# Performance work log

Hardware: AMD Instinct MI355X
Metric: run time of the kernel (lower is better)

## Reference

```python
import math
import jax, jax.numpy as jnp
import numpy as np

L, H = 4, 8  # num_layers, num_heads
SPARSE_FACTOR = 0.1
NEG = -1e9


def _ln(x, g, b, eps=1e-5):
    m = jnp.mean(x, axis=-1, keepdims=True)
    v = jnp.mean(jnp.square(x - m), axis=-1, keepdims=True)
    return (x - m) * jax.lax.rsqrt(v + eps) * g + b


def _pos_enc(S, D):
    # sinusoidal PE, shape (S, 1, D) matching pe.unsqueeze(0).transpose(0,1)[:S]
    pos = np.arange(S, dtype=np.float32)[:, None]
    div = np.exp(np.arange(0, D, 2, dtype=np.float32) * (-math.log(10000.0) / D))
    pe = np.zeros((S, D), dtype=np.float32)
    pe[:, 0::2] = np.sin(pos * div)
    pe[:, 1::2] = np.cos(pos * div)
    return jnp.asarray(pe)[:, None, :]


def setup_inputs() -> dict:
    key = jax.random.key(0)
    B, S, I, D, F = 128, 512, 64, 512, 2048
    ks = jax.random.split(key, 10)
    w = lambda k, shape: jax.random.normal(k, shape, jnp.float32) * 0.02
    return {
        'x': jax.random.normal(ks[0], (B, S, I), jnp.float32),
        'W_in': w(ks[1], (I, D)), 'b_in': jnp.zeros((D,), jnp.float32),
        'ln1_g': jnp.ones((L, D), jnp.float32), 'ln1_b': jnp.zeros((L, D), jnp.float32),
        'Wq': w(ks[2], (L, D, D)), 'Wk': w(ks[3], (L, D, D)), 'Wv': w(ks[4], (L, D, D)),
        'Wo': w(ks[5], (L, D, D)), 'bo': jnp.zeros((L, D), jnp.float32),
        'ln2_g': jnp.ones((L, D), jnp.float32), 'ln2_b': jnp.zeros((L, D), jnp.float32),
        'W1': w(ks[6], (L, D, F)), 'b1': jnp.zeros((L, F), jnp.float32),
        'W2': w(ks[7], (L, F, D)), 'b2': jnp.zeros((L, D), jnp.float32),
        'lnf_g': jnp.ones((D,), jnp.float32), 'lnf_b': jnp.zeros((D,), jnp.float32),
    }


def reference(x, W_in, b_in, ln1_g, ln1_b, Wq, Wk, Wv, Wo, bo,
              ln2_g, ln2_b, W1, b1, W2, b2, lnf_g, lnf_b):
    B, S, _ = x.shape
    D = W_in.shape[1]
    dk = D // H
    # source: scores last dim == batch (view+transpose quirk); k = max(1, int(B*0.1))
    topk = max(1, int(B * SPARSE_FACTOR))
    h = jnp.swapaxes(x, 0, 1) @ W_in + b_in          # (S,B,D)
    h = h * math.sqrt(D) + _pos_enc(S, D)

    def heads(z, w):
        return jnp.swapaxes((z @ w).reshape(S, B, H, dk), 1, 2)  # (S,H,B,dk)

    def body(h, p):
        g1, bb1, wq, wk, wv, wo, bo_, g2, bb2, w1, b1_, w2, b2_ = p
        y = _ln(h, g1, bb1)
        q, k, v = heads(y, wq), heads(y, wk), heads(y, wv)
        scores = jnp.einsum('shbd,shcd->shbc', q, k) / math.sqrt(dk)  # (S,H,B,B)
        kth = jax.lax.top_k(scores, topk)[0][..., -1:]
        scores = jnp.where(scores >= kth, scores, NEG)  # top-k sparsification
        attn = jax.nn.softmax(scores, axis=-1)
        ctx = jnp.einsum('shbc,shcd->shbd', attn, v)
        ctx = jnp.swapaxes(ctx, 1, 2).reshape(S, B, D)
        h = ctx @ wo + bo_ + h                       # attn out + residual
        f = jax.nn.gelu(_ln(h, g2, bb2) @ w1 + b1_, approximate=False) @ w2 + b2_
        return h + f, None

    h, _ = jax.lax.scan(body, h, (ln1_g, ln1_b, Wq, Wk, Wv, Wo, bo,
                                  ln2_g, ln2_b, W1, b1, W2, b2))
    h = _ln(h, lnf_g, lnf_b)
    return jnp.swapaxes(h, 0, 1)                     # (B,S,D)
```

## Files before the change

kernel.cpp:

```cpp
#include <hip/hip_runtime.h>
#include <math.h>

#define S_ 512
#define B_ 128
#define D_ 512
#define I_ 64
#define F_ 2048
#define H_ 8
#define DK_ 64
#define L_ 4
#define SB_ (S_*B_)

typedef unsigned short u16;
typedef unsigned int u32;
typedef __attribute__((ext_vector_type(4))) unsigned int u32x4;
typedef __attribute__((ext_vector_type(4))) float f32x4;

__device__ __forceinline__ u16 f2bf(float f){
  u32 x = __builtin_bit_cast(u32, f);
  x += 0x7fffu + ((x >> 16) & 1u);
  return (u16)(x >> 16);
}

__device__ __forceinline__ void mfma16(f32x4& c, const u32x4& a, const u32x4& b){
  asm volatile("v_mfma_f32_16x16x32_bf16 %0, %1, %2, %0" : "+v"(c) : "v"(a), "v"(b));
}

__device__ __forceinline__ void gload16(const u16* g, u16* l){
  __builtin_amdgcn_global_load_lds((const __attribute__((address_space(1))) unsigned int*)g,
                                   (__attribute__((address_space(3))) unsigned int*)l, 16, 0, 0);
}

__global__ void pe_kernel(float* __restrict__ pe){
  int s = blockIdx.x, d = threadIdx.x;
  float e = expf((float)(d & ~1) * (-9.210340371976184f / (float)D_));
  float arg = (float)s * e;
  pe[s*D_ + d] = (d & 1) ? cosf(arg) : sinf(arg);
}

__global__ void transpose_bf16(const float* __restrict__ src, u16* __restrict__ dst,
                               int R, int C, size_t zstride){
  __shared__ float t[32][33];
  size_t sbase = (size_t)blockIdx.z * R * C;
  size_t dbase = (size_t)blockIdx.z * zstride;
  int r0 = blockIdx.y*32, c0 = blockIdx.x*32;
  int tx = threadIdx.x, ty = threadIdx.y;
  #pragma unroll
  for (int j=0;j<4;j++)
    t[ty+j*8][tx] = src[sbase + (size_t)(r0+ty+j*8)*C + c0+tx];
  __syncthreads();
  #pragma unroll
  for (int j=0;j<4;j++)
    dst[dbase + (size_t)(c0+ty+j*8)*R + r0+tx] = f2bf(t[tx][ty+j*8]);
}

__global__ __launch_bounds__(512) void inproj_kernel(const float* __restrict__ x,
    const float* __restrict__ Win, const float* __restrict__ bin,
    const float* __restrict__ pe, float* __restrict__ h){
  __shared__ float xs[8][64];
  int t = threadIdx.x;
  float w[64];
  #pragma unroll
  for (int i=0;i<64;i++) w[i] = Win[i*D_ + t];
  float bd = bin[t];
  int r0 = blockIdx.x * 128;
  for (int batch=0; batch<16; batch++){
    int rb = r0 + batch*8;
    {
      int rr = t >> 6, i = t & 63;
      int r = rb + rr;
      int s = r >> 7, b = r & 127;
      xs[rr][i] = x[((size_t)b*S_ + s)*I_ + i];
    }
    __syncthreads();
    float acc[8];
    #pragma unroll
    for (int rr=0;rr<8;rr++) acc[rr] = 0.f;
    #pragma unroll
    for (int i4=0;i4<16;i4++){
      f32x4 xv[8];
      #pragma unroll
      for (int rr=0;rr<8;rr++) xv[rr] = *(const f32x4*)&xs[rr][i4*4];
      #pragma unroll
      for (int rr=0;rr<8;rr++){
        acc[rr] = fmaf(xv[rr][0], w[i4*4+0], acc[rr]);
        acc[rr] = fmaf(xv[rr][1], w[i4*4+1], acc[rr]);
        acc[rr] = fmaf(xv[rr][2], w[i4*4+2], acc[rr]);
        acc[rr] = fmaf(xv[rr][3], w[i4*4+3], acc[rr]);
      }
    }
    #pragma unroll
    for (int rr=0;rr<8;rr++){
      int r = rb + rr;
      int s = r >> 7;
      h[(size_t)r*D_ + t] = (acc[rr] + bd) * 22.627416997969522f + pe[s*D_ + t];
    }
    __syncthreads();
  }
}

template<int FINAL>
__global__ __launch_bounds__(256) void ln_kernel(const float* __restrict__ hsrc,
    const float* __restrict__ g, const float* __restrict__ bb,
    u16* __restrict__ outb, float* __restrict__ outf){
  int row = blockIdx.x*4 + (threadIdx.x>>6);
  int lane = threadIdx.x & 63;
  const float* hr = hsrc + (size_t)row*D_ + lane*8;
  f32x4 a0 = *(const f32x4*)hr;
  f32x4 a1 = *(const f32x4*)(hr+4);
  float v[8];
  #pragma unroll
  for (int j=0;j<4;j++){ v[j]=a0[j]; v[4+j]=a1[j]; }
  float sum = 0.f;
  #pragma unroll
  for (int j=0;j<8;j++) sum += v[j];
  #pragma unroll
  for (int m=1;m<64;m<<=1) sum += __shfl_xor(sum, m);
  float mean = sum * (1.f/(float)D_);
  float s2 = 0.f;
  #pragma unroll
  for (int j=0;j<8;j++){ float dd = v[j]-mean; s2 = fmaf(dd,dd,s2); }
  #pragma unroll
  for (int m=1;m<64;m<<=1) s2 += __shfl_xor(s2, m);
  float inv = rsqrtf(s2*(1.f/(float)D_) + 1e-5f);
  f32x4 g0 = *(const f32x4*)&g[lane*8];
  f32x4 g1 = *(const f32x4*)&g[lane*8+4];
  f32x4 b0 = *(const f32x4*)&bb[lane*8];
  f32x4 b1 = *(const f32x4*)&bb[lane*8+4];
  float o[8];
  #pragma unroll
  for (int j=0;j<4;j++){
    o[j]   = (v[j]-mean)*inv*g0[j] + b0[j];
    o[4+j] = (v[4+j]-mean)*inv*g1[j] + b1[j];
  }
  if (FINAL == 0){
    u32x4 pk;
    #pragma unroll
    for (int j=0;j<4;j++)
      pk[j] = (u32)f2bf(o[2*j]) | ((u32)f2bf(o[2*j+1])<<16);
    *(u32x4*)&outb[(size_t)row*D_ + lane*8] = pk;
  } else {
    int s = row>>7, b = row&(B_-1);
    float* op = outf + ((size_t)b*S_ + s)*D_ + lane*8;
    f32x4 r0, r1;
    #pragma unroll
    for (int j=0;j<4;j++){ r0[j]=o[j]; r1[j]=o[4+j]; }
    *(f32x4*)op = r0;
    *(f32x4*)(op+4) = r1;
  }
}

template<int MODE>
__global__ __launch_bounds__(256) void gemm_kernel(const u16* __restrict__ A,
    const u16* __restrict__ Wt, const float* __restrict__ bias,
    float* __restrict__ hres, u16* __restrict__ outb, int N, int K){
  const u32 nwg = gridDim.x * gridDim.y;
  u32 wg = blockIdx.y * gridDim.x + blockIdx.x;
  wg = (wg & 7) * (nwg >> 3) + (wg >> 3);
  const int m0 = (int)(wg / gridDim.x) * 128;
  const int n0 = (int)(wg % gridDim.x) * 128;
  __shared__ u16 a_lds[128*32];
  __shared__ u16 b_lds[128*32];
  const int t = threadIdx.x;
  const int lane = t & 63, wave = t >> 6;
  const int wm = wave >> 1, wn = wave & 1;
  const int rsel = lane & 15, kg = (lane>>4)*8;
  const u16* ag = A  + (size_t)(m0 + (t>>2))*K + (t&3)*8;
  const u16* bg = Wt + (size_t)(n0 + (t>>2))*K + (t&3)*8;
  f32x4 acc[4][4] = {};
  for (int k0 = 0; k0 < K; k0 += 32){
    asm volatile("s_nop 7\n\ts_nop 7");
    __syncthreads();
    gload16(ag + k0,                &a_lds[t*8]);
    gload16(ag + 64*(size_t)K + k0, &a_lds[2048 + t*8]);
    gload16(bg + k0,                &b_lds[t*8]);
    gload16(bg + 64*(size_t)K + k0, &b_lds[2048 + t*8]);
    __syncthreads();
    u32x4 af[4], bfr[4];
    #pragma unroll
    for (int i=0;i<4;i++){
      af[i]  = *(const u32x4*)&a_lds[(wm*64 + i*16 + rsel)*32 + kg];
      bfr[i] = *(const u32x4*)&b_lds[(wn*64 + i*16 + rsel)*32 + kg];
    }
    #pragma unroll
    for (int i=0;i<4;i++)
      #pragma unroll
      for (int j=0;j<4;j++)
        mfma16(acc[i][j], af[i], bfr[j]);
  }
  asm volatile("s_nop 7\n\ts_nop 7");
  const int rb = (lane>>4)*4;
  #pragma unroll
  for (int i=0;i<4;i++){
    #pragma unroll
    for (int j=0;j<4;j++){
      int gn = n0 + wn*64 + j*16 + rsel;
      #pragma unroll
      for (int rg=0;rg<4;rg++){
        int gr = m0 + wm*64 + i*16 + rb + rg;
        float val = acc[i][j][rg];
        if (MODE == 0){
          int mat = gn >> 9;
          int hh = (gn >> 6) & 7, dd = gn & 63;
          int s = gr >> 7, b = gr & 127;
          u16* dst = outb + (size_t)mat*33554432ull;
          dst[(size_t)((s*H_ + hh)*B_ + b)*DK_ + dd] = f2bf(val);
        } else if (MODE == 1){
          hres[(size_t)gr*D_ + gn] += val + bias[gn];
        } else {
          float xg = val + bias[gn];
          float ge = 0.5f*xg*(1.f + erff(xg*0.7071067811865476f));
          outb[(size_t)gr*(size_t)N + gn] = f2bf(ge);
        }
      }
    }
  }
}

__global__ __launch_bounds__(256, 2) void attn_kernel(const u16* __restrict__ qb,
    const u16* __restrict__ kb, const u16* __restrict__ vb, u16* __restrict__ cb){
  __shared__ __align__(16) char smem[80384];
  u16* q_lds = (u16*)smem;
  u16* k_lds = (u16*)(smem + 18432);
  float* S   = (float*)smem;
  u16* P     = (u16*)smem;
  u16* vT    = (u16*)(smem + 34816);
  u32* wl    = (u32*)(smem + 67584);
  float* rs  = (float*)(smem + 79872);
  int sh = blockIdx.x;
  int s = sh >> 3, hh = sh & 7;
  int t = threadIdx.x, lane = t & 63, wave = t >> 6;
  const u16* qg = qb + (size_t)sh * (B_*DK_);
  const u16* kg = kb + (size_t)sh * (B_*DK_);
  const u16* vg = vb + (size_t)sh * (B_*DK_);
  #pragma unroll
  for (int rr=0; rr<4; rr++){
    int idx = rr*2048 + t*8;
    int row = idx >> 6, col = idx & 63;
    *(u32x4*)&q_lds[row*72+col] = *(const u32x4*)&qg[idx];
    *(u32x4*)&k_lds[row*72+col] = *(const u32x4*)&kg[idx];
  }
  __syncthreads();
  int wm = wave>>1, wn = wave&1, rsel = lane & 15;
  f32x4 sacc[4][4] = {};
  #pragma unroll
  for (int ks=0; ks<2; ks++){
    asm volatile("s_nop 7\n\ts_nop 7");
    int ko = ks*32 + (lane>>4)*8;
    u32x4 qf[4], kf[4];
    #pragma unroll
    for (int i=0;i<4;i++){
      qf[i] = *(const u32x4*)&q_lds[(wm*64+i*16+rsel)*72 + ko];
      kf[i] = *(const u32x4*)&k_lds[(wn*64+i*16+rsel)*72 + ko];
    }
    #pragma unroll
    for (int i=0;i<4;i++)
      #pragma unroll
      for (int j=0;j<4;j++)
        mfma16(sacc[i][j], qf[i], kf[j]);
  }
  asm volatile("s_nop 7\n\ts_nop 7");
  __syncthreads();
  int rb = (lane>>4)*4;
  #pragma unroll
  for (int i=0;i<4;i++)
    #pragma unroll
    for (int j=0;j<4;j++)
      #pragma unroll
      for (int rg=0;rg<4;rg++)
        S[(wm*64+i*16+rb+rg)*132 + wn*64+j*16+rsel] = sacc[i][j][rg] * 0.125f;
  __syncthreads();
  int r = t >> 1, half = t & 1;
  const f32x4* srow4 = (const f32x4*)(S + r*132 + half*64);
  float kv[12];
  #pragma unroll
  for (int i=0;i<12;i++) kv[i] = -3.4e38f;
  for (int i4=0;i4<16;i4++){
    f32x4 v4 = srow4[i4];
    float m4 = fmaxf(fmaxf(v4[0],v4[1]), fmaxf(v4[2],v4[3]));
    if (m4 > kv[11]){
      #pragma unroll
      for (int z=0; z<4; z++){
        float inc = v4[z];
        if (inc > kv[11]){
          #pragma unroll
          for (int p=0;p<12;p++){
            float cur = kv[p];
            bool gt = inc > cur;
            kv[p] = gt ? inc : cur;
            inc   = gt ? cur : inc;
          }
        }
      }
    }
  }
  float kth = 3.4e38f;
  #pragma unroll
  for (int i=0;i<12;i++){
    float pb = __shfl_xor(kv[11-i], 1);
    kth = fminf(kth, fmaxf(kv[i], pb));
  }
  float mx = fmaxf(kv[0], __shfl_xor(kv[0], 1));
  float sum = 0.f;
  int n = 0;
  u32* myw = wl + t*12;
  for (int i4=0;i4<16;i4++){
    f32x4 v4 = srow4[i4];
    #pragma unroll
    for (int z=0; z<4; z++){
      float v = v4[z];
      if (v >= kth && n < 12){
        float e = __expf(v - mx);
        sum += e;
        myw[n] = ((u32)f2bf(e) << 16) | (u32)(half*64 + i4*4 + z);
        n++;
      }
    }
  }
  float tsum = sum + __shfl_xor(sum, 1);
  if (!half) rs[r] = 1.f / tsum;
  __syncthreads();
  {
    u32x4 zz = {0u,0u,0u,0u};
    #pragma unroll
    for (int z=0; z<9; z++){
      int idx = z*256 + t;
      if (idx < 2176) ((u32x4*)P)[idx] = zz;
    }
  }
  #pragma unroll
  for (int rr=0; rr<16; rr++){
    int idx2 = (rr*256 + t)*2;
    u32 u = *(const u32*)&vg[idx2];
    int c = idx2 >> 6, d0 = idx2 & 63;
    vT[d0*136 + c]     = (u16)(u & 0xffffu);
    vT[(d0+1)*136 + c] = (u16)(u >> 16);
  }
  __syncthreads();
  u16* prow = P + r*136;
  for (int j=0; j<n; j++){
    u32 e = myw[j];
    prow[e & 0xffffu] = (u16)(e >> 16);
  }
  __syncthreads();
  f32x4 cacc[4][2] = {};
  #pragma unroll
  for (int ks=0; ks<4; ks++){
    asm volatile("s_nop 7\n\ts_nop 7");
    int ko = ks*32 + (lane>>4)*8;
    u32x4 pf[4], vf[2];
    #pragma unroll
    for (int i=0;i<4;i++) pf[i] = *(const u32x4*)&P[(wm*64+i*16+rsel)*136 + ko];
    #pragma unroll
    for (int j=0;j<2;j++) vf[j] = *(const u32x4*)&vT[(wn*32+j*16+rsel)*136 + ko];
    #pragma unroll
    for (int i=0;i<4;i++)
      #pragma unroll
      for (int j=0;j<2;j++)
        mfma16(cacc[i][j], pf[i], vf[j]);
  }
  asm volatile("s_nop 7\n\ts_nop 7");
  #pragma unroll
  for (int i=0;i<4;i++)
    #pragma unroll
    for (int j=0;j<2;j++)
      #pragma unroll
      for (int rg=0;rg<4;rg++){
        int m = wm*64 + i*16 + rb + rg;
        int nn = wn*32 + j*16 + rsel;
        float val = cacc[i][j][rg] * rs[m];
        cb[((size_t)(s*B_ + m))*D_ + hh*DK_ + nn] = f2bf(val);
      }
}

extern "C" void kernel_launch(void* const* d_in, const int* in_sizes, int n_in,
                              void* d_out, int out_size, void* d_ws, size_t ws_size,
                              hipStream_t stream) {
  const float* x    = (const float*)d_in[0];
  const float* Win  = (const float*)d_in[1];
  const float* bin  = (const float*)d_in[2];
  const float* ln1g = (const float*)d_in[3];
  const float* ln1b = (const float*)d_in[4];
  const float* Wq   = (const float*)d_in[5];
  const float* Wk   = (const float*)d_in[6];
  const float* Wv   = (const float*)d_in[7];
  const float* Wo   = (const float*)d_in[8];
  const float* bo   = (const float*)d_in[9];
  const float* ln2g = (const float*)d_in[10];
  const float* ln2b = (const float*)d_in[11];
  const float* W1   = (const float*)d_in[12];
  const float* b1   = (const float*)d_in[13];
  const float* W2   = (const float*)d_in[14];
  const float* b2   = (const float*)d_in[15];
  const float* lnfg = (const float*)d_in[16];
  const float* lnfb = (const float*)d_in[17];

  char* ws = (char*)d_ws;
  float* h  = (float*)(ws);
  u16* yb   = (u16*)(ws + 134217728ull);
  u16* qb   = (u16*)(ws + 201326592ull);
  u16* kb   = (u16*)(ws + 268435456ull);
  u16* vb   = (u16*)(ws + 335544320ull);
  u16* cb   = (u16*)(ws + 402653184ull);
  u16* act  = qb;
  u16* wqkvT= (u16*)(ws + 469762048ull);
  u16* woT  = (u16*)(ws + 476053504ull);
  u16* w1T  = (u16*)(ws + 478150656ull);
  u16* w2T  = (u16*)(ws + 486539264ull);
  float* pe = (float*)(ws + 494927872ull);

  dim3 tb(32,8);
  pe_kernel<<<S_, D_, 0, stream>>>(pe);
  transpose_bf16<<<dim3(D_/32, D_/32, L_), tb, 0, stream>>>(Wq, wqkvT,            D_, D_, (size_t)3*D_*D_);
  transpose_bf16<<<dim3(D_/32, D_/32, L_), tb, 0, stream>>>(Wk, wqkvT + D_*D_,    D_, D_, (size_t)3*D_*D_);
  transpose_bf16<<<dim3(D_/32, D_/32, L_), tb, 0, stream>>>(Wv, wqkvT + 2*D_*D_,  D_, D_, (size_t)3*D_*D_);
  transpose_bf16<<<dim3(D_/32, D_/32, L_), tb, 0, stream>>>(Wo, woT,              D_, D_, (size_t)D_*D_);
  transpose_bf16<<<dim3(F_/32, D_/32, L_), tb, 0, stream>>>(W1, w1T, D_, F_, (size_t)D_*F_);
  transpose_bf16<<<dim3(D_/32, F_/32, L_), tb, 0, stream>>>(W2, w2T, F_, D_, (size_t)F_*D_);
  inproj_kernel<<<512, 512, 0, stream>>>(x, Win, bin, pe, h);

  for (int l=0; l<L_; l++){
    ln_kernel<0><<<SB_/4, 256, 0, stream>>>(h, ln1g + l*D_, ln1b + l*D_, yb, nullptr);
    gemm_kernel<0><<<dim3(12,512), 256, 0, stream>>>(yb, wqkvT + (size_t)l*3*D_*D_, nullptr, nullptr, qb, 1536, D_);
    attn_kernel<<<S_*H_, 256, 0, stream>>>(qb, kb, vb, cb);
    gemm_kernel<1><<<dim3(4,512), 256, 0, stream>>>(cb, woT + (size_t)l*D_*D_, bo + l*D_, h, nullptr, D_, D_);
    ln_kernel<0><<<SB_/4, 256, 0, stream>>>(h, ln2g + l*D_, ln2b + l*D_, yb, nullptr);
    gemm_kernel<2><<<dim3(16,512), 256, 0, stream>>>(yb, w1T + (size_t)l*D_*F_, b1 + l*F_, nullptr, act, F_, D_);
    gemm_kernel<1><<<dim3(4,512), 256, 0, stream>>>(act, w2T + (size_t)l*F_*D_, b2 + l*D_, h, nullptr, D_, F_);
  }
  ln_kernel<1><<<SB_/4, 256, 0, stream>>>(h, lnfg, lnfb, nullptr, (float*)d_out);
}
```

Before: 3.664 ms.

## Replace 128x128 GEMM with 256x256 tile, 8 waves, multi-buffered LDS pipeline

Rewrites the bf16 GEMM kernel to use 256x256 output tiles with 512 threads (8 waves, each covering 128x64), and a 4-slot LDS ring buffer that prefetches two k-steps ahead. The A and B global loads are interleaved with the two MFMA phases, using raw barriers, vmcnt waits and s_setprio. The goal is to hide global-load latency and raise arithmetic intensity per LDS byte. The cost is much larger LDS use (128KB per block) and more registers, which lowers occupancy, plus fewer workgroups per launch.

Result: no change. 3.607 ms (-1.5%).

```diff
diff --git a/kernel.cpp b/kernel.cpp
--- a/kernel.cpp
+++ b/kernel.cpp
@@ -151,53 +151,80 @@
 }
 
 template<int MODE>
-__global__ __launch_bounds__(256) void gemm_kernel(const u16* __restrict__ A,
+__global__ __launch_bounds__(512, 2) void gemm256(const u16* __restrict__ A,
     const u16* __restrict__ Wt, const float* __restrict__ bias,
     float* __restrict__ hres, u16* __restrict__ outb, int N, int K){
   const u32 nwg = gridDim.x * gridDim.y;
   u32 wg = blockIdx.y * gridDim.x + blockIdx.x;
   wg = (wg & 7) * (nwg >> 3) + (wg >> 3);
-  const int m0 = (int)(wg / gridDim.x) * 128;
-  const int n0 = (int)(wg % gridDim.x) * 128;
-  __shared__ u16 a_lds[128*32];
-  __shared__ u16 b_lds[128*32];
+  const int m0 = (int)(wg / gridDim.x) * 256;
+  const int n0 = (int)(wg % gridDim.x) * 256;
+  __shared__ u16 lds[4][2][256*32];
   const int t = threadIdx.x;
   const int lane = t & 63, wave = t >> 6;
-  const int wm = wave >> 1, wn = wave & 1;
-  const int rsel = lane & 15, kg = (lane>>4)*8;
+  const int wm = wave >> 2, wn = wave & 3;
+  const int rsel = lane & 15, kb = (lane>>4)*8;
   const u16* ag = A  + (size_t)(m0 + (t>>2))*K + (t&3)*8;
   const u16* bg = Wt + (size_t)(n0 + (t>>2))*K + (t&3)*8;
-  f32x4 acc[4][4] = {};
-  for (int k0 = 0; k0 < K; k0 += 32){
-    asm volatile("s_nop 7\n\ts_nop 7");
-    __syncthreads();
-    gload16(ag + k0,                &a_lds[t*8]);
-    gload16(ag + 64*(size_t)K + k0, &a_lds[2048 + t*8]);
-    gload16(bg + k0,                &b_lds[t*8]);
-    gload16(bg + 64*(size_t)K + k0, &b_lds[2048 + t*8]);
-    __syncthreads();
-    u32x4 af[4], bfr[4];
-    #pragma unroll
-    for (int i=0;i<4;i++){
-      af[i]  = *(const u32x4*)&a_lds[(wm*64 + i*16 + rsel)*32 + kg];
-      bfr[i] = *(const u32x4*)&b_lds[(wn*64 + i*16 + rsel)*32 + kg];
-    }
+  const int NT = K >> 5;
+  auto stageA = [&](int kt){
+    u16* dst = &lds[kt & 3][0][t*8];
+    gload16(ag + kt*32,                  dst);
+    gload16(ag + 128*(size_t)K + kt*32,  dst + 4096);
+  };
+  auto stageB = [&](int kt){
+    u16* dst = &lds[kt & 3][1][t*8];
+    gload16(bg + kt*32,                  dst);
+    gload16(bg + 128*(size_t)K + kt*32,  dst + 4096);
+  };
+  f32x4 acc[8][4] = {};
+  stageA(0); stageB(0); stageA(1); stageB(1);
+  asm volatile("s_waitcnt vmcnt(4)" ::: "memory");
+  __builtin_amdgcn_s_barrier();
+  for (int kt = 0; kt < NT; ++kt){
+    const u16* abuf = &lds[kt & 3][0][0];
+    const u16* bbuf = &lds[kt & 3][1][0];
+    u32x4 af[4], bf[4];
+    #pragma unroll
+    for (int i=0;i<4;i++) af[i] = *(const u32x4*)&abuf[(wm*128 + i*16 + rsel)*32 + kb];
+    #pragma unroll
+    for (int j=0;j<4;j++) bf[j] = *(const u32x4*)&bbuf[(wn*64 + j*16 + rsel)*32 + kb];
+    if (kt + 2 < NT) stageA(kt+2);
+    __builtin_amdgcn_s_barrier();
+    __builtin_amdgcn_s_setprio(1);
     #pragma unroll
     for (int i=0;i<4;i++)
       #pragma unroll
       for (int j=0;j<4;j++)
-        mfma16(acc[i][j], af[i], bfr[j]);
+        mfma16(acc[i][j], af[i], bf[j]);
+    __builtin_amdgcn_s_setprio(0);
+    __builtin_amdgcn_s_barrier();
+    u32x4 af2[4];
+    #pragma unroll
+    for (int i=0;i<4;i++) af2[i] = *(const u32x4*)&abuf[(wm*128 + 64 + i*16 + rsel)*32 + kb];
+    if (kt + 2 < NT) stageB(kt+2);
+    __builtin_amdgcn_s_barrier();
+    __builtin_amdgcn_s_setprio(1);
+    #pragma unroll
+    for (int i=0;i<4;i++)
+      #pragma unroll
+      for (int j=0;j<4;j++)
+        mfma16(acc[4+i][j], af2[i], bf[j]);
+    __builtin_amdgcn_s_setprio(0);
+    if (kt < NT-2) asm volatile("s_waitcnt vmcnt(4)" ::: "memory");
+    else           asm volatile("s_waitcnt vmcnt(0)" ::: "memory");
+    __builtin_amdgcn_s_barrier();
   }
   asm volatile("s_nop 7\n\ts_nop 7");
   const int rb = (lane>>4)*4;
   #pragma unroll
-  for (int i=0;i<4;i++){
+  for (int i=0;i<8;i++){
     #pragma unroll
     for (int j=0;j<4;j++){
       int gn = n0 + wn*64 + j*16 + rsel;
       #pragma unroll
       for (int rg=0;rg<4;rg++){
-        int gr = m0 + wm*64 + i*16 + rb + rg;
+        int gr = m0 + wm*128 + i*16 + rb + rg;
         float val = acc[i][j][rg];
         if (MODE == 0){
           int mat = gn >> 9;
@@ -421,12 +448,12 @@
 
   for (int l=0; l<L_; l++){
     ln_kernel<0><<<SB_/4, 256, 0, stream>>>(h, ln1g + l*D_, ln1b + l*D_, yb, nullptr);
-    gemm_kernel<0><<<dim3(12,512), 256, 0, stream>>>(yb, wqkvT + (size_t)l*3*D_*D_, nullptr, nullptr, qb, 1536, D_);
+    gemm256<0><<<dim3(6,256), 512, 0, stream>>>(yb, wqkvT + (size_t)l*3*D_*D_, nullptr, nullptr, qb, 1536, D_);
     attn_kernel<<<S_*H_, 256, 0, stream>>>(qb, kb, vb, cb);
-    gemm_kernel<1><<<dim3(4,512), 256, 0, stream>>>(cb, woT + (size_t)l*D_*D_, bo + l*D_, h, nullptr, D_, D_);
+    gemm256<1><<<dim3(2,256), 512, 0, stream>>>(cb, woT + (size_t)l*D_*D_, bo + l*D_, h, nullptr, D_, D_);
     ln_kernel<0><<<SB_/4, 256, 0, stream>>>(h, ln2g + l*D_, ln2b + l*D_, yb, nullptr);
-    gemm_kernel<2><<<dim3(16,512), 256, 0, stream>>>(yb, w1T + (size_t)l*D_*F_, b1 + l*F_, nullptr, act, F_, D_);
-    gemm_kernel<1><<<dim3(4,512), 256, 0, stream>>>(act, w2T + (size_t)l*F_*D_, b2 + l*D_, h, nullptr, D_, F_);
+    gemm256<2><<<dim3(8,256), 512, 0, stream>>>(yb, w1T + (size_t)l*D_*F_, b1 + l*F_, nullptr, act, F_, D_);
+    gemm256<1><<<dim3(2,256), 512, 0, stream>>>(act, w2T + (size_t)l*F_*D_, b2 + l*D_, h, nullptr, D_, F_);
   }
   ln_kernel<1><<<SB_/4, 256, 0, stream>>>(h, lnfg, lnfb, nullptr, (float*)d_out);
 }
```

## Fuse residual GEMMs with following LayerNorm, swizzle LDS, use tanh GELU

Applied to the files above, without the earlier changes.

Adds a gemmLN kernel that computes a full 128x512 output row block per workgroup. It applies bias and the residual add into h, then computes the LayerNorm for the next stage in the epilogue and writes the bf16 normalized activations. This removes the separate LN kernels and one full read of h per LN. The GEMM LDS layout gets an XOR swizzle to cut bank conflicts. The exact erf GELU is replaced by a tanh approximation, which changes numerics slightly. The fused kernel has a 512-column N tile with far fewer workgroups (512), so occupancy and parallelism are reduced.

Result: slower. 3.975 ms (+8.5%).

```diff
diff --git a/kernel.cpp b/kernel.cpp
--- a/kernel.cpp
+++ b/kernel.cpp
@@ -29,6 +29,14 @@
 __device__ __forceinline__ void gload16(const u16* g, u16* l){
   __builtin_amdgcn_global_load_lds((const __attribute__((address_space(1))) unsigned int*)g,
                                    (__attribute__((address_space(3))) unsigned int*)l, 16, 0, 0);
+}
+
+__device__ __forceinline__ float gelu_fast(float x){
+  float u = 0.7978845608028654f * fmaf(0.044715f*x*x, x, x);
+  float ae = __expf(-2.f*fabsf(u));
+  float th = (1.f - ae) / (1.f + ae);
+  th = (u < 0.f) ? -th : th;
+  return 0.5f * x * (1.f + th);
 }
 
 __global__ void pe_kernel(float* __restrict__ pe){
@@ -151,9 +159,9 @@
 }
 
 template<int MODE>
-__global__ __launch_bounds__(256) void gemm_kernel(const u16* __restrict__ A,
+__global__ __launch_bounds__(256) void gemm128(const u16* __restrict__ A,
     const u16* __restrict__ Wt, const float* __restrict__ bias,
-    float* __restrict__ hres, u16* __restrict__ outb, int N, int K){
+    u16* __restrict__ outb, int N, int K){
   const u32 nwg = gridDim.x * gridDim.y;
   u32 wg = blockIdx.y * gridDim.x + blockIdx.x;
   wg = (wg & 7) * (nwg >> 3) + (wg >> 3);
@@ -164,9 +172,11 @@
   const int t = threadIdx.x;
   const int lane = t & 63, wave = t >> 6;
   const int wm = wave >> 1, wn = wave & 1;
-  const int rsel = lane & 15, kg = (lane>>4)*8;
-  const u16* ag = A  + (size_t)(m0 + (t>>2))*K + (t&3)*8;
-  const u16* bg = Wt + (size_t)(n0 + (t>>2))*K + (t&3)*8;
+  const int rsel = lane & 15;
+  const int kswz = (((lane>>4) ^ ((rsel>>1)&3)) * 8);
+  const int sslot = (t&3) ^ ((t>>3)&3);
+  const u16* ag = A  + (size_t)(m0 + (t>>2))*K + sslot*8;
+  const u16* bg = Wt + (size_t)(n0 + (t>>2))*K + sslot*8;
   f32x4 acc[4][4] = {};
   for (int k0 = 0; k0 < K; k0 += 32){
     asm volatile("s_nop 7\n\ts_nop 7");
@@ -179,8 +189,8 @@
     u32x4 af[4], bfr[4];
     #pragma unroll
     for (int i=0;i<4;i++){
-      af[i]  = *(const u32x4*)&a_lds[(wm*64 + i*16 + rsel)*32 + kg];
-      bfr[i] = *(const u32x4*)&b_lds[(wn*64 + i*16 + rsel)*32 + kg];
+      af[i]  = *(const u32x4*)&a_lds[(wm*64 + i*16 + rsel)*32 + kswz];
+      bfr[i] = *(const u32x4*)&b_lds[(wn*64 + i*16 + rsel)*32 + kswz];
     }
     #pragma unroll
     for (int i=0;i<4;i++)
@@ -205,12 +215,126 @@
           int s = gr >> 7, b = gr & 127;
           u16* dst = outb + (size_t)mat*33554432ull;
           dst[(size_t)((s*H_ + hh)*B_ + b)*DK_ + dd] = f2bf(val);
-        } else if (MODE == 1){
-          hres[(size_t)gr*D_ + gn] += val + bias[gn];
         } else {
-          float xg = val + bias[gn];
-          float ge = 0.5f*xg*(1.f + erff(xg*0.7071067811865476f));
-          outb[(size_t)gr*(size_t)N + gn] = f2bf(ge);
+          outb[(size_t)gr*(size_t)N + gn] = f2bf(gelu_fast(val + bias[gn]));
+        }
+      }
+    }
+  }
+}
+
+__global__ __launch_bounds__(512, 2) void gemmLN(const u16* __restrict__ A,
+    const u16* __restrict__ Wt, const float* __restrict__ bias,
+    float* __restrict__ hres, u16* __restrict__ yb,
+    const float* __restrict__ gamma, const float* __restrict__ beta, int K){
+  const int m0 = blockIdx.x * 128;
+  __shared__ u16 a_lds[128*32];
+  __shared__ u16 b_lds[512*32];
+  __shared__ float part_sum[128][4];
+  __shared__ float part_sq[128][4];
+  const int t = threadIdx.x;
+  const int lane = t & 63, wave = t >> 6;
+  const int wm = wave >> 2, wn = wave & 3;
+  const int rsel = lane & 15;
+  const int kswz = (((lane>>4) ^ ((rsel>>1)&3)) * 8);
+  const int sslot = (t&3) ^ ((t>>3)&3);
+  const u16* ag = A  + (size_t)(m0 + (t>>7))*K + sslot*8;
+  const u16* ag2 = A + (size_t)(m0 + (t>>2))*K + sslot*8;
+  const u16* bg  = Wt + (size_t)(t>>2)*K + sslot*8;
+  (void)ag;
+  f32x4 acc[4][8] = {};
+  for (int k0 = 0; k0 < K; k0 += 32){
+    asm volatile("s_nop 7\n\ts_nop 7");
+    __syncthreads();
+    gload16(ag2 + k0, &a_lds[t*8]);
+    #pragma unroll
+    for (int li=0; li<4; li++)
+      gload16(bg + (size_t)li*128*K + k0, &b_lds[li*4096 + t*8]);
+    __syncthreads();
+    u32x4 af[4], bf[8];
+    #pragma unroll
+    for (int i=0;i<4;i++) af[i] = *(const u32x4*)&a_lds[(wm*64 + i*16 + rsel)*32 + kswz];
+    #pragma unroll
+    for (int j=0;j<8;j++) bf[j] = *(const u32x4*)&b_lds[(wn*128 + j*16 + rsel)*32 + kswz];
+    #pragma unroll
+    for (int i=0;i<4;i++)
+      #pragma unroll
+      for (int j=0;j<8;j++)
+        mfma16(acc[i][j], af[i], bf[j]);
+  }
+  asm volatile("s_nop 7\n\ts_nop 7");
+  const int rb = (lane>>4)*4;
+  float bs[8];
+  #pragma unroll
+  for (int j=0;j<8;j++) bs[j] = bias[wn*128 + j*16 + rsel];
+  float sums[4][4], sqs[4][4];
+  #pragma unroll
+  for (int i=0;i<4;i++)
+    #pragma unroll
+    for (int rg=0;rg<4;rg++){ sums[i][rg]=0.f; sqs[i][rg]=0.f; }
+  #pragma unroll
+  for (int i=0;i<4;i++){
+    #pragma unroll
+    for (int rg=0;rg<4;rg++){
+      int gr = m0 + wm*64 + i*16 + rb + rg;
+      float* hrow = hres + (size_t)gr*D_;
+      #pragma unroll
+      for (int j=0;j<8;j++){
+        int gc = wn*128 + j*16 + rsel;
+        float v = acc[i][j][rg] + bs[j] + hrow[gc];
+        hrow[gc] = v;
+        acc[i][j][rg] = v;
+        sums[i][rg] += v;
+        sqs[i][rg] = fmaf(v, v, sqs[i][rg]);
+      }
+    }
+  }
+  if (gamma){
+    #pragma unroll
+    for (int i=0;i<4;i++)
+      #pragma unroll
+      for (int rg=0;rg<4;rg++){
+        #pragma unroll
+        for (int m=1;m<16;m<<=1){
+          sums[i][rg] += __shfl_xor(sums[i][rg], m);
+          sqs[i][rg]  += __shfl_xor(sqs[i][rg],  m);
+        }
+      }
+    __syncthreads();
+    if (rsel == 0){
+      #pragma unroll
+      for (int i=0;i<4;i++)
+        #pragma unroll
+        for (int rg=0;rg<4;rg++){
+          int r = wm*64 + i*16 + rb + rg;
+          part_sum[r][wn] = sums[i][rg];
+          part_sq[r][wn]  = sqs[i][rg];
+        }
+    }
+    __syncthreads();
+    float gs[8], bbs[8];
+    #pragma unroll
+    for (int j=0;j<8;j++){
+      gs[j]  = gamma[wn*128 + j*16 + rsel];
+      bbs[j] = beta [wn*128 + j*16 + rsel];
+    }
+    #pragma unroll
+    for (int i=0;i<4;i++){
+      #pragma unroll
+      for (int rg=0;rg<4;rg++){
+        int r = wm*64 + i*16 + rb + rg;
+        float s  = part_sum[r][0] + part_sum[r][1] + part_sum[r][2] + part_sum[r][3];
+        float q  = part_sq[r][0]  + part_sq[r][1]  + part_sq[r][2]  + part_sq[r][3];
+        float mean = s * (1.f/(float)D_);
+        float var  = fmaxf(q * (1.f/(float)D_) - mean*mean, 0.f);
+        float inv  = rsqrtf(var + 1e-5f);
+        int gr = m0 + r;
+        u16* yrow = yb + (size_t)gr*D_;
+        #pragma unroll
+        for (int j=0;j<8;j++){
+          int gc = wn*128 + j*16 + rsel;
+          float o = (acc[i][j][rg] - mean)*inv*gs[j] + bbs[j];
+          yrow[gc] = f2bf(o);
         }
       }
     }
@@ -419,14 +543,17 @@
   transpose_bf16<<<dim3(D_/32, F_/32, L_), tb, 0, stream>>>(W2, w2T, F_, D_, (size_t)F_*D_);
   inproj_kernel<<<512, 512, 0, stream>>>(x, Win, bin, pe, h);
 
+  ln_kernel<0><<<SB_/4, 256, 0, stream>>>(h, ln1g, ln1b, yb, nullptr);
   for (int l=0; l<L_; l++){
-    ln_kernel<0><<<SB_/4, 256, 0, stream>>>(h, ln1g + l*D_, ln1b + l*D_, yb, nullptr);
-    gemm_kernel<0><<<dim3(12,512), 256, 0, stream>>>(yb, wqkvT + (size_t)l*3*D_*D_, nullptr, nullptr, qb, 1536, D_);
+    gemm128<0><<<dim3(12,512), 256, 0, stream>>>(yb, wqkvT + (size_t)l*3*D_*D_, nullptr, qb, 1536, D_);
     attn_kernel<<<S_*H_, 256, 0, stream>>>(qb, kb, vb, cb);
-    gemm_kernel<1><<<dim3(4,512), 256, 0, stream>>>(cb, woT + (size_t)l*D_*D_, bo + l*D_, h, nullptr, D_, D_);
-    ln_kernel<0><<<SB_/4, 256, 0, stream>>>(h, ln2g + l*D_, ln2b + l*D_, yb, nullptr);
-    gemm_kernel<2><<<dim3(16,512), 256, 0, stream>>>(yb, w1T + (size_t)l*D_*F_, b1 + l*F_, nullptr, act, F_, D_);
-    gemm_kernel<1><<<dim3(4,512), 256, 0, stream>>>(act, w2T + (size_t)l*F_*D_, b2 + l*D_, h, nullptr, D_, F_);
+    gemmLN<<<512, 512, 0, stream>>>(cb, woT + (size_t)l*D_*D_, bo + l*D_, h, yb,
+                                    ln2g + l*D_, ln2b + l*D_, D_);
+    gemm128<2><<<dim3(16,512), 256, 0, stream>>>(yb, w1T + (size_t)l*D_*F_, b1 + l*F_, act, F_, D_);
+    const float* g1n = (l < L_-1) ? (ln1g + (l+1)*D_) : nullptr;
+    const float* b1n = (l < L_-1) ? (ln1b + (l+1)*D_) : nullptr;
+    gemmLN<<<512, 512, 0, stream>>>(act, w2T + (size_t)l*F_*D_, b2 + l*D_, h, yb,
+                                    g1n, b1n, F_);
   }
   ln_kernel<1><<<SB_/4, 256, 0, stream>>>(h, lnfg, lnfb, nullptr, (float*)d_out);
 }
```

## Double GEMM K-tile to 64 with XOR-swizzled LDS and tanh GELU

Applied to the files above, without the earlier changes.

The GEMM kernel now stages 64-wide K tiles instead of 32, which halves the number of barrier-synchronised load steps per output tile. It uses an XOR swizzle on the LDS layout to avoid bank conflicts when reading MFMA fragments. The exact erf GELU in the FFN epilogue is replaced by the tanh approximation built on a fast exp, which changes numerics slightly relative to the exact-GELU reference. The LN launch moves to the end of the previous layer, an equivalent reordering.

After: 3.505 ms. 4.3% less time.

```diff
diff --git a/kernel.cpp b/kernel.cpp
--- a/kernel.cpp
+++ b/kernel.cpp
@@ -29,6 +29,14 @@
 __device__ __forceinline__ void gload16(const u16* g, u16* l){
   __builtin_amdgcn_global_load_lds((const __attribute__((address_space(1))) unsigned int*)g,
                                    (__attribute__((address_space(3))) unsigned int*)l, 16, 0, 0);
+}
+
+__device__ __forceinline__ float gelu_fast(float x){
+  float u = 0.7978845608028654f * fmaf(0.044715f*x*x, x, x);
+  float ae = __expf(-2.f*fabsf(u));
+  float th = (1.f - ae) / (1.f + ae);
+  th = (u < 0.f) ? -th : th;
+  return 0.5f * x * (1.f + th);
 }
 
 __global__ void pe_kernel(float* __restrict__ pe){
@@ -151,7 +159,7 @@
 }
 
 template<int MODE>
-__global__ __launch_bounds__(256) void gemm_kernel(const u16* __restrict__ A,
+__global__ __launch_bounds__(256) void gemm128(const u16* __restrict__ A,
     const u16* __restrict__ Wt, const float* __restrict__ bias,
     float* __restrict__ hres, u16* __restrict__ outb, int N, int K){
   const u32 nwg = gridDim.x * gridDim.y;
@@ -159,28 +167,42 @@
   wg = (wg & 7) * (nwg >> 3) + (wg >> 3);
   const int m0 = (int)(wg / gridDim.x) * 128;
   const int n0 = (int)(wg % gridDim.x) * 128;
-  __shared__ u16 a_lds[128*32];
-  __shared__ u16 b_lds[128*32];
+  __shared__ u16 a_lds[128*64];
+  __shared__ u16 b_lds[128*64];
   const int t = threadIdx.x;
   const int lane = t & 63, wave = t >> 6;
   const int wm = wave >> 1, wn = wave & 1;
-  const int rsel = lane & 15, kg = (lane>>4)*8;
-  const u16* ag = A  + (size_t)(m0 + (t>>2))*K + (t&3)*8;
-  const u16* bg = Wt + (size_t)(n0 + (t>>2))*K + (t&3)*8;
+  const int rsel = lane & 15;
+  const int kp0 = (((lane>>4)    ) ^ (rsel&7)) * 8;
+  const int kp1 = (((lane>>4) | 4) ^ (rsel&7)) * 8;
+  const int sl = (t&7) ^ ((t>>3)&7);
+  const u16* ag = A  + (size_t)(m0 + (t>>3))*K + sl*8;
+  const u16* bg = Wt + (size_t)(n0 + (t>>3))*K + sl*8;
   f32x4 acc[4][4] = {};
-  for (int k0 = 0; k0 < K; k0 += 32){
+  for (int k0 = 0; k0 < K; k0 += 64){
     asm volatile("s_nop 7\n\ts_nop 7");
     __syncthreads();
-    gload16(ag + k0,                &a_lds[t*8]);
-    gload16(ag + 64*(size_t)K + k0, &a_lds[2048 + t*8]);
-    gload16(bg + k0,                &b_lds[t*8]);
-    gload16(bg + 64*(size_t)K + k0, &b_lds[2048 + t*8]);
+    #pragma unroll
+    for (int p=0;p<4;p++){
+      gload16(ag + (size_t)(p*32)*K + k0, &a_lds[p*2048 + t*8]);
+      gload16(bg + (size_t)(p*32)*K + k0, &b_lds[p*2048 + t*8]);
+    }
     __syncthreads();
     u32x4 af[4], bfr[4];
     #pragma unroll
     for (int i=0;i<4;i++){
-      af[i]  = *(const u32x4*)&a_lds[(wm*64 + i*16 + rsel)*32 + kg];
-      bfr[i] = *(const u32x4*)&b_lds[(wn*64 + i*16 + rsel)*32 + kg];
+      af[i]  = *(const u32x4*)&a_lds[(wm*64 + i*16 + rsel)*64 + kp0];
+      bfr[i] = *(const u32x4*)&b_lds[(wn*64 + i*16 + rsel)*64 + kp0];
+    }
+    #pragma unroll
+    for (int i=0;i<4;i++)
+      #pragma unroll
+      for (int j=0;j<4;j++)
+        mfma16(acc[i][j], af[i], bfr[j]);
+    #pragma unroll
+    for (int i=0;i<4;i++){
+      af[i]  = *(const u32x4*)&a_lds[(wm*64 + i*16 + rsel)*64 + kp1];
+      bfr[i] = *(const u32x4*)&b_lds[(wn*64 + i*16 + rsel)*64 + kp1];
     }
     #pragma unroll
     for (int i=0;i<4;i++)
@@ -208,9 +230,7 @@
         } else if (MODE == 1){
           hres[(size_t)gr*D_ + gn] += val + bias[gn];
         } else {
-          float xg = val + bias[gn];
-          float ge = 0.5f*xg*(1.f + erff(xg*0.7071067811865476f));
-          outb[(size_t)gr*(size_t)N + gn] = f2bf(ge);
+          outb[(size_t)gr*(size_t)N + gn] = f2bf(gelu_fast(val + bias[gn]));
         }
       }
     }
@@ -419,14 +439,16 @@
   transpose_bf16<<<dim3(D_/32, F_/32, L_), tb, 0, stream>>>(W2, w2T, F_, D_, (size_t)F_*D_);
   inproj_kernel<<<512, 512, 0, stream>>>(x, Win, bin, pe, h);
 
+  ln_kernel<0><<<SB_/4, 256, 0, stream>>>(h, ln1g, ln1b, yb, nullptr);
   for (int l=0; l<L_; l++){
-    ln_kernel<0><<<SB_/4, 256, 0, stream>>>(h, ln1g + l*D_, ln1b + l*D_, yb, nullptr);
-    gemm_kernel<0><<<dim3(12,512), 256, 0, stream>>>(yb, wqkvT + (size_t)l*3*D_*D_, nullptr, nullptr, qb, 1536, D_);
+    gemm128<0><<<dim3(12,512), 256, 0, stream>>>(yb, wqkvT + (size_t)l*3*D_*D_, nullptr, nullptr, qb, 1536, D_);
     attn_kernel<<<S_*H_, 256, 0, stream>>>(qb, kb, vb, cb);
-    gemm_kernel<1><<<dim3(4,512), 256, 0, stream>>>(cb, woT + (size_t)l*D_*D_, bo + l*D_, h, nullptr, D_, D_);
+    gemm128<1><<<dim3(4,512), 256, 0, stream>>>(cb, woT + (size_t)l*D_*D_, bo + l*D_, h, nullptr, D_, D_);
     ln_kernel<0><<<SB_/4, 256, 0, stream>>>(h, ln2g + l*D_, ln2b + l*D_, yb, nullptr);
-    gemm_kernel<2><<<dim3(16,512), 256, 0, stream>>>(yb, w1T + (size_t)l*D_*F_, b1 + l*F_, nullptr, act, F_, D_);
-    gemm_kernel<1><<<dim3(4,512), 256, 0, stream>>>(act, w2T + (size_t)l*F_*D_, b2 + l*D_, h, nullptr, D_, F_);
+    gemm128<2><<<dim3(16,512), 256, 0, stream>>>(yb, w1T + (size_t)l*D_*F_, b1 + l*F_, nullptr, act, F_, D_);
+    gemm128<1><<<dim3(4,512), 256, 0, stream>>>(act, w2T + (size_t)l*F_*D_, b2 + l*D_, h, nullptr, D_, F_);
+    if (l < L_-1)
+      ln_kernel<0><<<SB_/4, 256, 0, stream>>>(h, ln1g + (l+1)*D_, ln1b + (l+1)*D_, yb, nullptr);
   }
   ln_kernel<1><<<SB_/4, 256, 0, stream>>>(h, lnfg, lnfb, nullptr, (float*)d_out);
 }
```
